# Kernel optimization log

Measured on AMD Instinct MI355X. Metric: run time of the kernel, lower is better.

## Reference

```python
import jax, jax.numpy as jnp
import numpy as np

# Model hyperparameters (match init_kwargs)
T = 3          # reasoning hops
L = 3          # rule channels (parallel LSTMs)
E = 50000      # number of entities
N = 1000000    # number of KG triples
R = 200        # r_size = (n-1)//2
NREL = 2 * R + 1  # n = 401 (forward rels, inverse rels, identity)
H = 256        # emb_size
TAU = 10.0     # tau_1 softmax temperature
TOPK = 1000    # top-k state pruning for hops t>=1
B = 8          # batch size


def setup_inputs() -> dict:
    key = jax.random.key(0)
    ks = jax.random.split(key, 16)
    s = 0.05
    return {
        "input_x": jax.random.randint(ks[0], (B,), 0, E),
        "input_r": jax.random.randint(ks[1], (B,), 0, NREL),
        "e2triple": jax.random.randint(ks[2], (3, N), 0, E),
        "triple2e": jax.random.randint(ks[3], (2, N), 0, E),
        "r2triple": jax.random.randint(ks[4], (1, N), 0, R),
        "emb": jax.random.normal(ks[5], (NREL, H), jnp.float32) * s,
        "Wih_f": jax.random.normal(ks[6], (L, 4 * H, H), jnp.float32) * s,
        "Whh_f": jax.random.normal(ks[7], (L, 4 * H, H), jnp.float32) * s,
        "bih_f": jax.random.normal(ks[8], (L, 4 * H), jnp.float32) * s,
        "bhh_f": jax.random.normal(ks[9], (L, 4 * H), jnp.float32) * s,
        "Wih_b": jax.random.normal(ks[10], (L, 4 * H, H), jnp.float32) * s,
        "Whh_b": jax.random.normal(ks[11], (L, 4 * H, H), jnp.float32) * s,
        "bih_b": jax.random.normal(ks[12], (L, 4 * H), jnp.float32) * s,
        "bhh_b": jax.random.normal(ks[13], (L, 4 * H), jnp.float32) * s,
        "linW": jax.random.normal(ks[14], (NREL, 2 * H), jnp.float32) * s,
        "linb": jax.random.normal(ks[15], (NREL,), jnp.float32) * s,
    }


def _lstm_scan(x, Wih, Whh, bih, bhh):
    # x: [S, B, H]; PyTorch gate order i, f, g, o. Returns hidden seq [S, B, H].
    Bn = x.shape[1]
    Hh = Whh.shape[1]
    pre = x @ Wih.T + bih + bhh  # hoist input projection out of the scan

    def step(carry, xt):
        h, c = carry
        g = xt + h @ Whh.T
        i, f, gg, o = jnp.split(g, 4, axis=-1)
        c = jax.nn.sigmoid(f) * c + jax.nn.sigmoid(i) * jnp.tanh(gg)
        h = jax.nn.sigmoid(o) * jnp.tanh(c)
        return (h, c), h

    init = (jnp.zeros((Bn, Hh), x.dtype), jnp.zeros((Bn, Hh), x.dtype))
    _, hs = jax.lax.scan(step, init, pre)
    return hs


def reference(input_x, input_r, e2triple, triple2e, r2triple, emb,
              Wih_f, Whh_f, bih_f, bhh_f, Wih_b, Whh_b, bih_b, bhh_b,
              linW, linb):
    Bsz = input_x.shape[0]
    x0 = jax.nn.one_hot(input_x, E, dtype=emb.dtype)  # [B, E] one-hot query entity
    q = emb[input_r]                                   # [B, H] query relation emb
    # [T+1, B, H]: T copies of the query rel emb, last step is the special emb[-1]
    seq = jnp.concatenate([
        jnp.broadcast_to(q[None], (T, Bsz, H)),
        jnp.broadcast_to(emb[-1][None, None, :], (1, Bsz, H)),
    ], axis=0)

    outs = []
    for l in range(L):  # small fixed number of structurally distinct LSTMs
        hf = _lstm_scan(seq, Wih_f[l], Whh_f[l], bih_f[l], bhh_f[l])
        hb = _lstm_scan(seq[::-1], Wih_b[l], Whh_b[l], bih_b[l], bhh_b[l])[::-1]
        rnn = jnp.concatenate([hf, hb], axis=-1).transpose(1, 0, 2)  # [B, T+1, 2H]
        outs.append(rnn[:, :-1] @ linW.T + linb)                      # [B, T, n]
    w_all = jnp.stack(outs, axis=2)  # [B, T, L, n]

    heads = e2triple[0]   # [N] head entity per triple
    tails = triple2e[1]   # [N] tail entity per triple
    tails2 = e2triple[2]  # [N] tail entity per triple (inverse-direction gather)
    rels = r2triple[0]    # [N] relation per triple, in [0, R)

    def propagate(x, w):
        # x: [B, *, E] entity state, w: [B, L, n] relation weights
        s_i = w[:, :, -1:] * x                              # identity relation
        msg_f = x[:, :, heads] * w[:, :, rels]              # [B, L, N] fwd messages
        s_h = jnp.zeros((Bsz, L, E), x.dtype).at[:, :, tails].add(msg_f)
        msg_b = x[:, :, tails2] * w[:, :, rels + R]         # inverse relations
        s_t = jnp.zeros((Bsz, L, E), x.dtype).at[:, :, heads].add(msg_b)
        return s_i + s_h + s_t

    def prune_topk(x, k):
        # keep top-k entity scores per (batch, channel), zero the rest
        th = jax.lax.top_k(x, k)[0][..., -1:]
        return jnp.where(x >= th, x, jnp.zeros((), x.dtype))

    s = None
    for t in range(T):
        w = jax.nn.softmax(w_all[:, t] / TAU, axis=-1)      # [B, L, n]
        xin = x0[:, None, :] if t == 0 else prune_topk(s, TOPK)
        st = propagate(xin, w)
        s = st / jnp.maximum(st.sum(-1, keepdims=True), 1e-7)
    return s.sum(axis=1)  # [B, E]
```

## Files before the change

kernel.cpp:

```cpp
#include <hip/hip_runtime.h>
#include <math.h>

#define TT 3
#define LL 3
#define EE 50000
#define NN 1000000
#define RR 200
#define NRELC 401
#define HH 256
#define BB 8
#define KTOP 1000
#define SROW 24
#define NBUCK 782
#define BSH 6
#define CSRN (2 * NN)
#define STB 512
#define SEGS 50176

__device__ __forceinline__ float sigmoidf_(float x) {
    if (x >= 0.f) { return 1.f / (1.f + expf(-x)); }
    float z = expf(x); return z / (1.f + z);
}

__global__ __launch_bounds__(256) void pre_kernel(
    const int* __restrict__ input_r, const float* __restrict__ emb,
    const float* __restrict__ Wih_f, const float* __restrict__ bih_f, const float* __restrict__ bhh_f,
    const float* __restrict__ Wih_b, const float* __restrict__ bih_b, const float* __restrict__ bhh_b,
    float* __restrict__ preq, float* __restrict__ pree)
{
    int wave = blockIdx.x * 4 + (threadIdx.x >> 6);
    if (wave >= 1536) return;
    int lane = threadIdx.x & 63;
    int row0 = wave * 4;
    int ld = row0 >> 10;
    int l = ld >> 1, dir = ld & 1;
    const float* Wih = (dir ? Wih_b : Wih_f) + (size_t)l * 4 * HH * HH;
    const float* bih = (dir ? bih_b : bih_f) + l * 4 * HH;
    const float* bhh = (dir ? bhh_b : bhh_f) + l * 4 * HH;

    float4 xf[9];
    for (int b = 0; b < 8; ++b) {
        int r = input_r[b];
        xf[b] = *(const float4*)(emb + (size_t)r * HH + lane * 4);
    }
    xf[8] = *(const float4*)(emb + (size_t)(NRELC - 1) * HH + lane * 4);

    for (int rr = 0; rr < 4; ++rr) {
        int row = (row0 + rr) & 1023;
        float4 w4 = *(const float4*)(Wih + (size_t)row * HH + lane * 4);
        float acc[9];
        #pragma unroll
        for (int c = 0; c < 9; ++c)
            acc[c] = w4.x * xf[c].x + w4.y * xf[c].y + w4.z * xf[c].z + w4.w * xf[c].w;
        #pragma unroll
        for (int off = 32; off > 0; off >>= 1)
            #pragma unroll
            for (int c = 0; c < 9; ++c) acc[c] += __shfl_xor(acc[c], off);
        float bsum = bih[row] + bhh[row];
        if (lane < 8) preq[((size_t)ld * 8 + lane) * 1024 + row] = acc[lane] + bsum;
        if (lane == 8) pree[(size_t)ld * 1024 + row] = acc[8] + bsum;
    }
}

__global__ __launch_bounds__(256) void rec_kernel(
    const float* __restrict__ Whh_f, const float* __restrict__ Whh_b,
    const float* __restrict__ preq, const float* __restrict__ pree,
    const float* __restrict__ hstate, float* __restrict__ gates, int step)
{
    int wave = blockIdx.x * 4 + (threadIdx.x >> 6);
    if (wave >= 1536) return;
    int lane = threadIdx.x & 63;
    int row0 = wave * 4;
    int ld = row0 >> 10;
    int l = ld >> 1, dir = ld & 1;
    const float* Whh = (dir ? Whh_b : Whh_f) + (size_t)l * 4 * HH * HH;
    bool use_e = dir ? (step == 0) : (step == 3);

    float4 hf[8];
    for (int b = 0; b < 8; ++b)
        hf[b] = *(const float4*)(hstate + ((size_t)ld * 8 + b) * HH + lane * 4);

    for (int rr = 0; rr < 4; ++rr) {
        int row = (row0 + rr) & 1023;
        float4 w4 = *(const float4*)(Whh + (size_t)row * HH + lane * 4);
        float acc[8];
        #pragma unroll
        for (int b = 0; b < 8; ++b)
            acc[b] = w4.x * hf[b].x + w4.y * hf[b].y + w4.z * hf[b].z + w4.w * hf[b].w;
        #pragma unroll
        for (int off = 32; off > 0; off >>= 1)
            #pragma unroll
            for (int b = 0; b < 8; ++b) acc[b] += __shfl_xor(acc[b], off);
        if (lane < 8) {
            float pre = use_e ? pree[(size_t)ld * 1024 + row]
                              : preq[((size_t)ld * 8 + lane) * 1024 + row];
            gates[((size_t)ld * 8 + lane) * 1024 + row] = acc[lane] + pre;
        }
    }
}

__global__ __launch_bounds__(256) void hupdate_kernel(
    const float* __restrict__ preq, const float* __restrict__ pree,
    const float* __restrict__ gates, float* __restrict__ hstate,
    float* __restrict__ cstate, float* __restrict__ hbuf2, int step)
{
    int g = blockIdx.x * 256 + threadIdx.x;
    int ld = g >> 11;
    int b = (g >> 8) & 7;
    int j = g & 255;
    int dir = ld & 1;
    bool use_e = dir ? (step == 0) : (step == 3);
    float gv[4];
    #pragma unroll
    for (int q = 0; q < 4; ++q) {
        int row = q * 256 + j;
        if (step == 0)
            gv[q] = use_e ? pree[(size_t)ld * 1024 + row]
                          : preq[((size_t)ld * 8 + b) * 1024 + row];
        else
            gv[q] = gates[((size_t)ld * 8 + b) * 1024 + row];
    }
    float c = (step == 0) ? 0.f : cstate[g];
    float iv = sigmoidf_(gv[0]), fv = sigmoidf_(gv[1]);
    float gg = tanhf(gv[2]),     ov = sigmoidf_(gv[3]);
    c = fv * c + iv * gg;
    float h = ov * tanhf(c);
    cstate[g] = c;
    hstate[g] = h;
    int t_out = dir ? (3 - step) : step;
    if (t_out <= 2) hbuf2[(((size_t)ld * 8 + b) * 3 + t_out) * HH + j] = h;
}

__global__ __launch_bounds__(256) void logits_dot(
    const float* __restrict__ hbuf2, const float* __restrict__ linW,
    const float* __restrict__ linb, float* __restrict__ wbuf)
{
    int wave = blockIdx.x * 4 + (threadIdx.x >> 6);
    if (wave >= 3 * 3 * NRELC) return;
    int lane = threadIdx.x & 63;
    int n = wave % NRELC;
    int tc = wave / NRELC;
    int t = tc / 3, chunk = tc % 3;
    const float4* wr = (const float4*)(linW + (size_t)n * 2 * HH + lane * 8);
    float4 w4a = wr[0], w4b = wr[1];
    float acc[8];
    #pragma unroll
    for (int i = 0; i < 8; ++i) {
        int combo = chunk * 8 + i;
        int b = combo / 3, l = combo % 3;
        int ldh = (lane < 32) ? (l * 2 + 0) : (l * 2 + 1);
        const float* hsrc = hbuf2 + (((size_t)ldh * 8 + b) * 3 + t) * HH + (lane & 31) * 8;
        float4 f0 = *(const float4*)hsrc;
        float4 f1 = *(const float4*)(hsrc + 4);
        acc[i] = w4a.x * f0.x + w4a.y * f0.y + w4a.z * f0.z + w4a.w * f0.w
               + w4b.x * f1.x + w4b.y * f1.y + w4b.z * f1.z + w4b.w * f1.w;
    }
    #pragma unroll
    for (int off = 32; off > 0; off >>= 1)
        #pragma unroll
        for (int i = 0; i < 8; ++i) acc[i] += __shfl_xor(acc[i], off);
    if (lane < 8) {
        int combo = chunk * 8 + lane;
        wbuf[((size_t)t * 24 + combo) * NRELC + n] = acc[lane] + linb[n];
    }
}

__global__ __launch_bounds__(256) void softmax_kernel(float* __restrict__ wbuf) {
    int rowi = blockIdx.x;
    float* w = wbuf + (size_t)rowi * NRELC;
    __shared__ float red[256];
    int tid = threadIdx.x;
    float v0 = w[tid];
    float v1 = (tid + 256 < NRELC) ? w[tid + 256] : -1e30f;
    red[tid] = fmaxf(v0, v1); __syncthreads();
    for (int s2 = 128; s2 > 0; s2 >>= 1) {
        if (tid < s2) red[tid] = fmaxf(red[tid], red[tid + s2]);
        __syncthreads();
    }
    float m = red[0]; __syncthreads();
    float e0 = expf((v0 - m) * 0.1f);
    float e1 = (tid + 256 < NRELC) ? expf((v1 - m) * 0.1f) : 0.f;
    red[tid] = e0 + e1; __syncthreads();
    for (int s2 = 128; s2 > 0; s2 >>= 1) {
        if (tid < s2) red[tid] += red[tid + s2];
        __syncthreads();
    }
    float denom = red[0];
    w[tid] = e0 / denom;
    if (tid + 256 < NRELC) w[tid + 256] = e1 / denom;
}

__global__ __launch_bounds__(256) void fill_seed(
    float* __restrict__ s, const int* __restrict__ input_x, const float* __restrict__ w0,
    unsigned* __restrict__ rowcnt)
{
    __shared__ int xs[8];
    __shared__ float wv[24];
    if (threadIdx.x < 8) xs[threadIdx.x] = input_x[threadIdx.x];
    if (threadIdx.x < 24) wv[threadIdx.x] = w0[(size_t)threadIdx.x * NRELC + (NRELC - 1)];
    if (blockIdx.x == 0 && threadIdx.x < 24) rowcnt[threadIdx.x] = 0u;
    __syncthreads();
    int i = blockIdx.x * 256 + threadIdx.x;
    if (i >= SROW * EE) return;
    int row = i % 24;
    int e = i / 24;
    s[i] = (e == xs[row / 3]) ? wv[row] : 0.f;
}

__global__ __launch_bounds__(256) void hop0_scan(
    const int* __restrict__ heads, const int* __restrict__ tails,
    const int* __restrict__ tails2, const int* __restrict__ rels,
    const int* __restrict__ input_x, const float* __restrict__ w0,
    float* __restrict__ s)
{
    __shared__ int xs[BB];
    if (threadIdx.x < BB) xs[threadIdx.x] = input_x[threadIdx.x];
    __syncthreads();
    int i = blockIdx.x * 256 + threadIdx.x;
    if (i >= NN) return;
    int h = heads[i], t2 = tails2[i];
    bool any = false;
    #pragma unroll
    for (int b = 0; b < BB; ++b) any = any || (h == xs[b]) || (t2 == xs[b]);
    if (!any) return;
    int tl = tails[i], rr = rels[i];
    for (int b = 0; b < BB; ++b) {
        if (h == xs[b])
            for (int l = 0; l < LL; ++l)
                atomicAdd(&s[(size_t)tl * SROW + b * 3 + l], w0[(b * 3 + l) * NRELC + rr]);
        if (t2 == xs[b])
            for (int l = 0; l < LL; ++l)
                atomicAdd(&s[(size_t)h * SROW + b * 3 + l], w0[(b * 3 + l) * NRELC + rr + RR]);
    }
}

__global__ __launch_bounds__(256) void rowsum_compact(
    const float* __restrict__ s, float* __restrict__ partial,
    unsigned* __restrict__ ckey, unsigned* __restrict__ rowcnt, int do_compact)
{
    __shared__ float acc[24];
    __shared__ unsigned lkey[24][168];
    __shared__ unsigned lcnt[24];
    __shared__ unsigned lbase[24];
    int tid = threadIdx.x;
    if (tid < 24) { acc[tid] = 0.f; lcnt[tid] = 0u; }
    __syncthreads();
    int gidx = blockIdx.x * 256 + tid;
    int row = gidx % 24;
    float a = 0.f;
    const int total = SROW * EE;
    for (int k0 = 0; k0 < 52; k0 += 13) {
        for (int kk = 0; kk < 13; ++kk) {
            long i = (long)gidx + (long)(k0 + kk) * 24576;
            if (i < total) {
                float v = s[i];
                a += v;
                if (do_compact && __float_as_uint(v) != 0u) {
                    unsigned slot = atomicAdd(&lcnt[row], 1u);
                    slot = min(slot, 167u);
                    lkey[row][slot] = __float_as_uint(v);
                }
            }
        }
        if (do_compact) {
            __syncthreads();
            if (tid < 24) {
                unsigned c = min(lcnt[tid], 168u);
                lcnt[tid] = c;
                lbase[tid] = min(atomicAdd(&rowcnt[tid], c), (unsigned)SEGS);
            }
            __syncthreads();
            int r = tid % 24;
            int nthr = (r < 16) ? 11 : 10;
            unsigned cnt = lcnt[r], base = lbase[r];
            if (base + cnt > (unsigned)SEGS) cnt = (unsigned)SEGS - base;
            for (unsigned j = (unsigned)(tid / 24); j < cnt; j += nthr)
                ckey[(size_t)r * SEGS + base + j] = lkey[r][j];
            __syncthreads();
            if (tid < 24) lcnt[tid] = 0u;
            __syncthreads();
        }
    }
    atomicAdd(&acc[row], a);
    __syncthreads();
    if (tid < 24) partial[blockIdx.x * 24 + tid] = acc[tid];
}

__global__ __launch_bounds__(256) void rowsum_fin(
    const float* __restrict__ partial, float* __restrict__ sums,
    const float* __restrict__ w_t, float* __restrict__ wsc,
    float* __restrict__ wTg)
{
    int r = blockIdx.x;
    int tid = threadIdx.x;
    __shared__ float sa;
    if (tid == 0) {
        float a = 0.f;
        for (int j = 0; j < 96; ++j) a += partial[j * 24 + r];
        a = fmaxf(a, 1e-7f);
        sums[r] = a;
        sa = a;
    }
    __syncthreads();
    if (w_t != nullptr) {
        float a = sa;
        for (int i = tid; i < NRELC; i += 256) {
            float v = w_t[(size_t)r * NRELC + i] / a;
            wsc[(size_t)r * NRELC + i] = v;
            if (wTg != nullptr && i < 2 * RR) wTg[(size_t)i * SROW + r] = v;
        }
    }
}

__global__ __launch_bounds__(256) void rowsum_fin2(
    const float* __restrict__ partial2, float* __restrict__ sums,
    const float* __restrict__ w_t, float* __restrict__ wsc,
    float* __restrict__ wTg)
{
    int r = blockIdx.x;
    int tid = threadIdx.x;
    __shared__ float red[256];
    float a = 0.f;
    for (int g = tid; g < NBUCK; g += 256) a += partial2[(size_t)g * 24 + r];
    red[tid] = a; __syncthreads();
    for (int s2 = 128; s2 > 0; s2 >>= 1) {
        if (tid < s2) red[tid] += red[tid + s2];
        __syncthreads();
    }
    __shared__ float sa;
    if (tid == 0) { sa = fmaxf(red[0], 1e-7f); sums[r] = sa; }
    __syncthreads();
    if (w_t != nullptr) {
        float aa = sa;
        for (int i = tid; i < NRELC; i += 256) {
            float v = w_t[(size_t)r * NRELC + i] / aa;
            wsc[(size_t)r * NRELC + i] = v;
            if (wTg != nullptr && i < 2 * RR) wTg[(size_t)i * SROW + r] = v;
        }
    }
}

__global__ __launch_bounds__(512) void topk_select(
    const unsigned* __restrict__ ckey, const unsigned* __restrict__ rowcnt,
    float* __restrict__ th, int* __restrict__ mask)
{
    int row = blockIdx.x, tid = threadIdx.x;
    {
        int per = (EE + 23) / 24;
        int e0 = row * per, e1 = min(e0 + per, EE);
        for (int e = e0 + tid; e < e1; e += 512) mask[e] = 0;
    }
    const unsigned* keys = ckey + (size_t)row * SEGS;
    int n = min((int)rowcnt[row], SEGS);
    __shared__ unsigned hist[256];
    __shared__ int red[256];
    __shared__ int sh_bin, sh_rem;
    unsigned prefix = 0;
    int remk = KTOP;
    int iters = (n + 511) / 512;
    int lane = tid & 63;
    for (int round = 0; round < 4; ++round) {
        if (tid < 256) hist[tid] = 0u;
        __syncthreads();
        int shift = 24 - 8 * round;
        for (int it = 0; it < iters; ++it) {
            int i = it * 512 + tid;
            bool valid = (i < n);
            unsigned key = valid ? keys[i] : 0u;
            valid = valid && (round == 0 || (key >> (shift + 8)) == prefix);
            unsigned bin = valid ? ((key >> shift) & 255u) : 0u;
            unsigned long long peers = __ballot(valid);
            #pragma unroll
            for (int bit = 0; bit < 8; ++bit) {
                unsigned long long bm = __ballot(valid && ((bin >> bit) & 1u));
                peers &= ((bin >> bit) & 1u) ? bm : ~bm;
            }
            if (valid) {
                unsigned long long lower = peers & ((1ull << lane) - 1ull);
                if (lower == 0ull)
                    atomicAdd(&hist[bin], (unsigned)__popcll(peers));
            }
        }
        __syncthreads();
        if (tid < 256) red[tid] = (int)hist[tid];
        __syncthreads();
        for (int off = 1; off < 256; off <<= 1) {
            int v = 0;
            if (tid < 256 && tid + off < 256) v = red[tid + off];
            __syncthreads();
            if (tid < 256) red[tid] += v;
            __syncthreads();
        }
        if (tid == 0) { sh_bin = 0; sh_rem = remk; }
        __syncthreads();
        if (tid < 256) {
            int cnt = (int)hist[tid];
            int above = (tid == 255) ? 0 : red[tid + 1];
            if (above < remk && above + cnt >= remk) { sh_bin = tid; sh_rem = remk - above; }
        }
        __syncthreads();
        prefix = (prefix << 8) | (unsigned)sh_bin;
        remk = sh_rem;
        __syncthreads();
    }
    if (tid == 0) th[row] = __uint_as_float(prefix);
}

__global__ __launch_bounds__(256) void prune_flat(
    float* __restrict__ s, const float* __restrict__ th,
    const float* __restrict__ wsc, float* __restrict__ x, int* __restrict__ mask,
    unsigned* __restrict__ rowcnt, int write_s)
{
    __shared__ float ths[24], w4s[24];
    if (threadIdx.x < 24) {
        ths[threadIdx.x] = th[threadIdx.x];
        w4s[threadIdx.x] = wsc[threadIdx.x * NRELC + (NRELC - 1)];
    }
    if (blockIdx.x == 0 && threadIdx.x < 24) rowcnt[threadIdx.x] = 0u;
    __syncthreads();
    int i = blockIdx.x * 256 + threadIdx.x;
    if (i >= SROW * EE) return;
    int row = i % 24;
    int e = i / 24;
    float v = s[i];
    float xv = (v >= ths[row]) ? v : 0.f;
    x[i] = xv;
    if (write_s) s[i] = w4s[row] * xv;
    if (xv > 0.f) atomicOr(&mask[e], 1 << (row / 3));
}

__global__ __launch_bounds__(256) void hop_scan(
    const int* __restrict__ heads, const int* __restrict__ tails,
    const int* __restrict__ tails2, const int* __restrict__ rels,
    const int* __restrict__ mask, const float* __restrict__ x,
    const float* __restrict__ wsc, float* __restrict__ s)
{
    int gid = blockIdx.x * 256 + threadIdx.x;
    int i = gid >> 3;
    if (i >= NN) return;
    int b = gid & 7;
    int h = heads[i], t2 = tails2[i];
    int mh = mask[h], mt = mask[t2];
    bool ah = (mh >> b) & 1;
    bool at = (mt >> b) & 1;
    if (!(ah || at)) return;
    int tl = tails[i], rr = rels[i];
    int row = b * 3;
    if (ah) {
        float v0 = x[(size_t)h * SROW + row];
        float v1 = x[(size_t)h * SROW + row + 1];
        float v2 = x[(size_t)h * SROW + row + 2];
        if (v0 != 0.f) atomicAdd(&s[(size_t)tl * SROW + row],     v0 * wsc[(row)     * NRELC + rr]);
        if (v1 != 0.f) atomicAdd(&s[(size_t)tl * SROW + row + 1], v1 * wsc[(row + 1) * NRELC + rr]);
        if (v2 != 0.f) atomicAdd(&s[(size_t)tl * SROW + row + 2], v2 * wsc[(row + 2) * NRELC + rr]);
    }
    if (at) {
        float v0 = x[(size_t)t2 * SROW + row];
        float v1 = x[(size_t)t2 * SROW + row + 1];
        float v2 = x[(size_t)t2 * SROW + row + 2];
        if (v0 != 0.f) atomicAdd(&s[(size_t)h * SROW + row],     v0 * wsc[(row)     * NRELC + rr + RR]);
        if (v1 != 0.f) atomicAdd(&s[(size_t)h * SROW + row + 1], v1 * wsc[(row + 1) * NRELC + rr + RR]);
        if (v2 != 0.f) atomicAdd(&s[(size_t)h * SROW + row + 2], v2 * wsc[(row + 2) * NRELC + rr + RR]);
    }
}

__global__ __launch_bounds__(256) void csr_hist(
    const int* __restrict__ heads, const int* __restrict__ tails,
    unsigned* __restrict__ bh)
{
    __shared__ unsigned h[NBUCK];
    int tid = threadIdx.x;
    for (int i = tid; i < NBUCK; i += 256) h[i] = 0u;
    __syncthreads();
    for (int i = blockIdx.x * 256 + tid; i < NN; i += STB * 256) {
        atomicAdd(&h[tails[i] >> BSH], 1u);
        atomicAdd(&h[heads[i] >> BSH], 1u);
    }
    __syncthreads();
    for (int j = tid; j < NBUCK; j += 256)
        bh[(size_t)j * STB + blockIdx.x] = h[j];
}

__global__ __launch_bounds__(512) void csr_scanb(
    unsigned* __restrict__ bh, unsigned* __restrict__ gcnt)
{
    __shared__ unsigned sc[STB];
    int bk = blockIdx.x, tid = threadIdx.x;
    unsigned v = bh[(size_t)bk * STB + tid];
    sc[tid] = v; __syncthreads();
    #pragma unroll
    for (int o = 1; o < STB; o <<= 1) {
        unsigned u = (tid >= o) ? sc[tid - o] : 0u;
        __syncthreads();
        sc[tid] += u;
        __syncthreads();
    }
    bh[(size_t)bk * STB + tid] = sc[tid] - v;
    if (tid == STB - 1) gcnt[bk] = sc[tid];
}

__global__ __launch_bounds__(1024) void csr_scan2(
    const unsigned* __restrict__ gcnt, unsigned* __restrict__ gOff)
{
    __shared__ unsigned sc[1024];
    int tid = threadIdx.x;
    unsigned v = (tid < NBUCK) ? gcnt[tid] : 0u;
    sc[tid] = v; __syncthreads();
    #pragma unroll
    for (int o = 1; o < 1024; o <<= 1) {
        unsigned u = (tid >= o) ? sc[tid - o] : 0u;
        __syncthreads();
        sc[tid] += u;
        __syncthreads();
    }
    if (tid < NBUCK) gOff[tid] = sc[tid] - v;
    if (tid == NBUCK - 1) gOff[NBUCK] = sc[tid];
}

__global__ __launch_bounds__(256) void csr_stage2(
    const int* __restrict__ heads, const int* __restrict__ tails,
    const int* __restrict__ tails2, const int* __restrict__ rels,
    const unsigned* __restrict__ gOff, const unsigned* __restrict__ bh,
    unsigned* __restrict__ staging)
{
    __shared__ unsigned base[NBUCK];
    __shared__ unsigned cur[NBUCK];
    int tid = threadIdx.x;
    for (int j = tid; j < NBUCK; j += 256) {
        base[j] = gOff[j] + bh[(size_t)j * STB + blockIdx.x];
        cur[j] = 0u;
    }
    __syncthreads();
    for (int i = blockIdx.x * 256 + tid; i < NN; i += STB * 256) {
        unsigned rl = (unsigned)rels[i];
        int h = heads[i], d1 = tails[i], t2 = tails2[i];
        unsigned p1 = base[d1 >> BSH] + atomicAdd(&cur[d1 >> BSH], 1u);
        if (p1 < (unsigned)CSRN)
            staging[p1] = ((unsigned)(d1 & 63) << 26) | ((unsigned)h << 9) | rl;
        unsigned p2 = base[h >> BSH] + atomicAdd(&cur[h >> BSH], 1u);
        if (p2 < (unsigned)CSRN)
            staging[p2] = ((unsigned)(h & 63) << 26) | ((unsigned)t2 << 9) | (rl + RR);
    }
}

__global__ __launch_bounds__(256) void hop_bucket(
    const unsigned* __restrict__ gOff, const unsigned* __restrict__ staging,
    const int* __restrict__ mask, const float* __restrict__ x,
    const float* __restrict__ wT, const float* __restrict__ wsc,
    float* __restrict__ s, float* __restrict__ partial2,
    unsigned* __restrict__ ckey, unsigned* __restrict__ rowcnt, int do_compact)
{
    __shared__ float sl[64][24];
    __shared__ float w4s[24];
    __shared__ float acc24[24];
    __shared__ unsigned lcnt[24];
    __shared__ unsigned lbase[24];
    __shared__ unsigned lkey[24][64];
    int bk = blockIdx.x, tid = threadIdx.x;
    for (int i = tid; i < 64 * 24; i += 256) ((float*)sl)[i] = 0.f;
    if (tid < 24) {
        w4s[tid] = wsc[tid * NRELC + (NRELC - 1)];
        acc24[tid] = 0.f;
        lcnt[tid] = 0u;
    }
    __syncthreads();
    unsigned j0 = gOff[bk], j1 = gOff[bk + 1];
    for (unsigned j = j0 + tid; j < j1; j += 256) {
        unsigned p = staging[j];
        int src = (int)((p >> 9) & 0xFFFFu);
        int m = mask[src];
        if (!m) continue;
        int dl = (int)(p >> 26);
        int rel = (int)(p & 511u);
        const float* xs = x + (size_t)src * SROW;
        const float* wr = wT + (size_t)rel * SROW;
        while (m) {
            int b = __ffs(m) - 1; m &= m - 1;
            int r = b * 3;
            atomicAdd(&sl[dl][r],     xs[r]     * wr[r]);
            atomicAdd(&sl[dl][r + 1], xs[r + 1] * wr[r + 1]);
            atomicAdd(&sl[dl][r + 2], xs[r + 2] * wr[r + 2]);
        }
    }
    __syncthreads();
    int e0 = bk * 64;
    for (int idx = tid; idx < 64 * 24; idx += 256) {
        int el = idx / 24, row = idx % 24;
        int e = e0 + el;
        if (e >= EE) continue;
        float v = sl[el][row] + w4s[row] * x[(size_t)e * SROW + row];
        s[(size_t)e * SROW + row] = v;
        atomicAdd(&acc24[row], v);
        if (do_compact && __float_as_uint(v) != 0u) {
            unsigned slot = atomicAdd(&lcnt[row], 1u);
            slot = min(slot, 63u);
            lkey[row][slot] = __float_as_uint(v);
        }
    }
    __syncthreads();
    if (tid < 24) partial2[(size_t)bk * 24 + tid] = acc24[tid];
    if (do_compact) {
        if (tid < 24) {
            unsigned c = min(lcnt[tid], 64u);
            lcnt[tid] = c;
            lbase[tid] = min(atomicAdd(&rowcnt[tid], c), (unsigned)SEGS);
        }
        __syncthreads();
        int r = tid % 24;
        int nthr = (r < 16) ? 11 : 10;
        unsigned cnt = lcnt[r], base = lbase[r];
        if (base + cnt > (unsigned)SEGS) cnt = (unsigned)SEGS - base;
        for (unsigned j = (unsigned)(tid / 24); j < cnt; j += nthr)
            ckey[(size_t)r * SEGS + base + j] = lkey[r][j];
    }
}

__global__ void final_kernel(const float* __restrict__ s, const float* __restrict__ sums,
                             float* __restrict__ out) {
    __shared__ float ss[24];
    if (threadIdx.x < 24) ss[threadIdx.x] = sums[threadIdx.x];
    __syncthreads();
    int e = blockIdx.x * 256 + threadIdx.x;
    if (e >= EE) return;
    const float* se = s + (size_t)e * SROW;
    #pragma unroll
    for (int b = 0; b < 8; ++b)
        out[(size_t)b * EE + e] = se[b * 3] / ss[b * 3]
                                + se[b * 3 + 1] / ss[b * 3 + 1]
                                + se[b * 3 + 2] / ss[b * 3 + 2];
}

extern "C" void kernel_launch(void* const* d_in, const int* in_sizes, int n_in,
                              void* d_out, int out_size, void* d_ws, size_t ws_size,
                              hipStream_t stream)
{
    const int*   input_x  = (const int*)d_in[0];
    const int*   input_r  = (const int*)d_in[1];
    const int*   e2triple = (const int*)d_in[2];
    const int*   triple2e = (const int*)d_in[3];
    const int*   r2triple = (const int*)d_in[4];
    const float* emb      = (const float*)d_in[5];
    const float* Wih_f    = (const float*)d_in[6];
    const float* Whh_f    = (const float*)d_in[7];
    const float* bih_f    = (const float*)d_in[8];
    const float* bhh_f    = (const float*)d_in[9];
    const float* Wih_b    = (const float*)d_in[10];
    const float* Whh_b    = (const float*)d_in[11];
    const float* bih_b    = (const float*)d_in[12];
    const float* bhh_b    = (const float*)d_in[13];
    const float* linW     = (const float*)d_in[14];
    const float* linb     = (const float*)d_in[15];

    const int* heads  = e2triple;
    const int* tails2 = e2triple + 2 * (size_t)NN;
    const int* tails  = triple2e + (size_t)NN;
    const int* rels   = r2triple;

    float* ws      = (float*)d_ws;
    float* hbuf    = ws;
    float* wbuf    = hbuf + 36864;
    float* xst     = wbuf + 28872;
    float* sst     = xst + 1200000;
    float* sums    = sst + 1200000;
    float* th      = sums + 24;
    int*   mask    = (int*)(th + 24);
    float* partial = (float*)(mask + EE);
    unsigned* rowcnt  = (unsigned*)(partial + 2304);
    float* partial2   = (float*)(rowcnt + 32);
    unsigned* ckey    = (unsigned*)(partial2 + NBUCK * 24);
    unsigned* bh      = ckey + 24 * (size_t)SEGS;
    unsigned* gcnt    = bh + (size_t)NBUCK * STB;
    unsigned* gOff    = gcnt + 784;
    unsigned* staging = gOff + 800;
    float*    wT      = (float*)(staging + CSRN);
    const size_t NEED = (size_t)((wT + 9600) - ws) * 4;
    const bool use_csr = (ws_size >= NEED);
    float* wsc    = hbuf;
    float* preq   = xst;
    float* pree   = preq + 49152;
    float* gates  = pree + 6144;
    float* hstate = gates + 49152;
    float* cstate = hstate + 12288;

    float* out = (float*)d_out;
    const int EBLK  = (EE + 255) / 256;
    const int SBLK  = (SROW * EE + 255) / 256;
    const int NBLK  = (NN + 255) / 256;
    const int N8BLK = (NN * 8) / 256;

    pre_kernel<<<384, 256, 0, stream>>>(input_r, emb, Wih_f, bih_f, bhh_f,
                                        Wih_b, bih_b, bhh_b, preq, pree);
    hupdate_kernel<<<48, 256, 0, stream>>>(preq, pree, gates, hstate, cstate, hbuf, 0);
    for (int s = 1; s <= 3; ++s) {
        rec_kernel<<<384, 256, 0, stream>>>(Whh_f, Whh_b, preq, pree, hstate, gates, s);
        hupdate_kernel<<<48, 256, 0, stream>>>(preq, pree, gates, hstate, cstate, hbuf, s);
    }
    logits_dot<<<903, 256, 0, stream>>>(hbuf, linW, linb, wbuf);
    softmax_kernel<<<72, 256, 0, stream>>>(wbuf);

    if (use_csr) {
        csr_hist<<<STB, 256, 0, stream>>>(heads, tails, bh);
        csr_scanb<<<NBUCK, 512, 0, stream>>>(bh, gcnt);
        csr_scan2<<<1, 1024, 0, stream>>>(gcnt, gOff);
        csr_stage2<<<STB, 256, 0, stream>>>(heads, tails, tails2, rels, gOff, bh, staging);
    }

    fill_seed<<<SBLK, 256, 0, stream>>>(sst, input_x, wbuf, rowcnt);
    hop0_scan<<<NBLK, 256, 0, stream>>>(heads, tails, tails2, rels, input_x, wbuf, sst);
    rowsum_compact<<<96, 256, 0, stream>>>(sst, partial, ckey, rowcnt, 1);
    rowsum_fin<<<24, 256, 0, stream>>>(partial, sums, wbuf + 1 * 24 * NRELC, wsc,
                                       use_csr ? wT : nullptr);

    for (int t = 1; t < TT; ++t) {
        topk_select<<<24, 512, 0, stream>>>(ckey, rowcnt, th, mask);
        prune_flat<<<SBLK, 256, 0, stream>>>(sst, th, wsc, xst, mask, rowcnt,
                                             use_csr ? 0 : 1);
        const float* w_next = (t + 1 < TT) ? (wbuf + (size_t)(t + 1) * 24 * NRELC) : nullptr;
        if (use_csr) {
            hop_bucket<<<NBUCK, 256, 0, stream>>>(gOff, staging, mask, xst, wT, wsc,
                                                  sst, partial2, ckey, rowcnt,
                                                  (t + 1 < TT) ? 1 : 0);
            rowsum_fin2<<<24, 256, 0, stream>>>(partial2, sums, w_next, wsc, wT);
        } else {
            hop_scan<<<N8BLK, 256, 0, stream>>>(heads, tails, tails2, rels, mask, xst, wsc, sst);
            rowsum_compact<<<96, 256, 0, stream>>>(sst, partial, ckey, rowcnt,
                                                   (t + 1 < TT) ? 1 : 0);
            rowsum_fin<<<24, 256, 0, stream>>>(partial, sums, w_next, wsc, nullptr);
        }
    }

    final_kernel<<<EBLK, 256, 0, stream>>>(sst, sums, out);
}
```

Before: 323.0 us.

## Fuse LSTM gate update into matvec kernels, merge CSR histogram, widen rowsum grid

The LSTM recurrence now computes all four gates of one hidden unit in a single wave and applies the cell/hidden update in the same kernel. This removes the separate hupdate launches and the gates buffer, and hidden state ping-pongs between two buffers. The CSR histogram runs as extra blocks of the pre-projection kernel so both share one launch. rowsum_compact moves to 384 blocks with a single compaction pass instead of 96 blocks with four passes, which makes the partial-sum reduction longer.

```diff
diff --git a/kernel.cpp b/kernel.cpp
--- a/kernel.cpp
+++ b/kernel.cpp
@@ -22,17 +22,35 @@
     float z = expf(x); return z / (1.f + z);
 }
 
-__global__ __launch_bounds__(256) void pre_kernel(
+__global__ __launch_bounds__(256) void pre_fused(
     const int* __restrict__ input_r, const float* __restrict__ emb,
     const float* __restrict__ Wih_f, const float* __restrict__ bih_f, const float* __restrict__ bhh_f,
     const float* __restrict__ Wih_b, const float* __restrict__ bih_b, const float* __restrict__ bhh_b,
-    float* __restrict__ preq, float* __restrict__ pree)
-{
+    float* __restrict__ preq, float* __restrict__ pree,
+    float* __restrict__ hstate, float* __restrict__ cstate, float* __restrict__ hbuf2,
+    const int* __restrict__ heads, const int* __restrict__ tails,
+    unsigned* __restrict__ bh, int do_hist)
+{
+    if (blockIdx.x >= 384) {
+        if (!do_hist) return;
+        __shared__ unsigned h[NBUCK];
+        int tid = threadIdx.x;
+        int bid = blockIdx.x - 384;
+        for (int i = tid; i < NBUCK; i += 256) h[i] = 0u;
+        __syncthreads();
+        for (int i = bid * 256 + tid; i < NN; i += STB * 256) {
+            atomicAdd(&h[tails[i] >> BSH], 1u);
+            atomicAdd(&h[heads[i] >> BSH], 1u);
+        }
+        __syncthreads();
+        for (int j = tid; j < NBUCK; j += 256)
+            bh[(size_t)j * STB + bid] = h[j];
+        return;
+    }
     int wave = blockIdx.x * 4 + (threadIdx.x >> 6);
-    if (wave >= 1536) return;
     int lane = threadIdx.x & 63;
-    int row0 = wave * 4;
-    int ld = row0 >> 10;
+    int ld = wave >> 8;
+    int j  = wave & 255;
     int l = ld >> 1, dir = ld & 1;
     const float* Wih = (dir ? Wih_b : Wih_f) + (size_t)l * 4 * HH * HH;
     const float* bih = (dir ? bih_b : bih_f) + l * 4 * HH;
@@ -45,8 +63,9 @@
     }
     xf[8] = *(const float4*)(emb + (size_t)(NRELC - 1) * HH + lane * 4);
 
-    for (int rr = 0; rr < 4; ++rr) {
-        int row = (row0 + rr) & 1023;
+    float g4[4], ge4[4];
+    for (int q = 0; q < 4; ++q) {
+        int row = q * 256 + j;
         float4 w4 = *(const float4*)(Wih + (size_t)row * HH + lane * 4);
         float acc[9];
         #pragma unroll
@@ -57,31 +76,44 @@
             #pragma unroll
             for (int c = 0; c < 9; ++c) acc[c] += __shfl_xor(acc[c], off);
         float bsum = bih[row] + bhh[row];
-        if (lane < 8) preq[((size_t)ld * 8 + lane) * 1024 + row] = acc[lane] + bsum;
-        if (lane == 8) pree[(size_t)ld * 1024 + row] = acc[8] + bsum;
-    }
-}
-
-__global__ __launch_bounds__(256) void rec_kernel(
+        g4[q]  = (lane < 8 ? acc[lane] : 0.f) + bsum;
+        ge4[q] = acc[8] + bsum;
+        if (lane < 8) preq[((size_t)ld * 8 + lane) * 1024 + row] = g4[q];
+        if (lane == 8) pree[(size_t)ld * 1024 + row] = ge4[q];
+    }
+    if (lane < 8) {
+        float gi, gg, go;
+        if (dir == 0) { gi = g4[0]; gg = g4[2]; go = g4[3]; }
+        else          { gi = ge4[0]; gg = ge4[2]; go = ge4[3]; }
+        float c = sigmoidf_(gi) * tanhf(gg);
+        float h = sigmoidf_(go) * tanhf(c);
+        int g = (ld * 8 + lane) * 256 + j;
+        cstate[g] = c;
+        hstate[g] = h;
+        if (dir == 0) hbuf2[(((size_t)ld * 8 + lane) * 3 + 0) * HH + j] = h;
+    }
+}
+
+__global__ __launch_bounds__(256) void rec_fused(
     const float* __restrict__ Whh_f, const float* __restrict__ Whh_b,
     const float* __restrict__ preq, const float* __restrict__ pree,
-    const float* __restrict__ hstate, float* __restrict__ gates, int step)
+    const float* __restrict__ hprev, float* __restrict__ hnext,
+    float* __restrict__ cstate, float* __restrict__ hbuf2, int step)
 {
     int wave = blockIdx.x * 4 + (threadIdx.x >> 6);
-    if (wave >= 1536) return;
     int lane = threadIdx.x & 63;
-    int row0 = wave * 4;
-    int ld = row0 >> 10;
+    int ld = wave >> 8, j = wave & 255;
     int l = ld >> 1, dir = ld & 1;
     const float* Whh = (dir ? Whh_b : Whh_f) + (size_t)l * 4 * HH * HH;
-    bool use_e = dir ? (step == 0) : (step == 3);
+    bool use_e = (dir == 0) && (step == 3);
 
     float4 hf[8];
     for (int b = 0; b < 8; ++b)
-        hf[b] = *(const float4*)(hstate + ((size_t)ld * 8 + b) * HH + lane * 4);
-
-    for (int rr = 0; rr < 4; ++rr) {
-        int row = (row0 + rr) & 1023;
+        hf[b] = *(const float4*)(hprev + ((size_t)ld * 8 + b) * HH + lane * 4);
+
+    float g4[4];
+    for (int q = 0; q < 4; ++q) {
+        int row = q * 256 + j;
         float4 w4 = *(const float4*)(Whh + (size_t)row * HH + lane * 4);
         float acc[8];
         #pragma unroll
@@ -94,41 +126,21 @@
         if (lane < 8) {
             float pre = use_e ? pree[(size_t)ld * 1024 + row]
                               : preq[((size_t)ld * 8 + lane) * 1024 + row];
-            gates[((size_t)ld * 8 + lane) * 1024 + row] = acc[lane] + pre;
-        }
-    }
-}
-
-__global__ __launch_bounds__(256) void hupdate_kernel(
-    const float* __restrict__ preq, const float* __restrict__ pree,
-    const float* __restrict__ gates, float* __restrict__ hstate,
-    float* __restrict__ cstate, float* __restrict__ hbuf2, int step)
-{
-    int g = blockIdx.x * 256 + threadIdx.x;
-    int ld = g >> 11;
-    int b = (g >> 8) & 7;
-    int j = g & 255;
-    int dir = ld & 1;
-    bool use_e = dir ? (step == 0) : (step == 3);
-    float gv[4];
-    #pragma unroll
-    for (int q = 0; q < 4; ++q) {
-        int row = q * 256 + j;
-        if (step == 0)
-            gv[q] = use_e ? pree[(size_t)ld * 1024 + row]
-                          : preq[((size_t)ld * 8 + b) * 1024 + row];
-        else
-            gv[q] = gates[((size_t)ld * 8 + b) * 1024 + row];
-    }
-    float c = (step == 0) ? 0.f : cstate[g];
-    float iv = sigmoidf_(gv[0]), fv = sigmoidf_(gv[1]);
-    float gg = tanhf(gv[2]),     ov = sigmoidf_(gv[3]);
-    c = fv * c + iv * gg;
-    float h = ov * tanhf(c);
-    cstate[g] = c;
-    hstate[g] = h;
-    int t_out = dir ? (3 - step) : step;
-    if (t_out <= 2) hbuf2[(((size_t)ld * 8 + b) * 3 + t_out) * HH + j] = h;
+            g4[q] = acc[lane] + pre;
+        }
+    }
+    if (lane < 8) {
+        int g = (ld * 8 + lane) * 256 + j;
+        float c = cstate[g];
+        float iv = sigmoidf_(g4[0]), fv = sigmoidf_(g4[1]);
+        float gg = tanhf(g4[2]),     ov = sigmoidf_(g4[3]);
+        c = fv * c + iv * gg;
+        float h = ov * tanhf(c);
+        cstate[g] = c;
+        hnext[g] = h;
+        int t_out = dir ? (3 - step) : step;
+        if (t_out <= 2) hbuf2[(((size_t)ld * 8 + lane) * 3 + t_out) * HH + j] = h;
+    }
 }
 
 __global__ __launch_bounds__(256) void logits_dot(
@@ -249,37 +261,33 @@
     int row = gidx % 24;
     float a = 0.f;
     const int total = SROW * EE;
-    for (int k0 = 0; k0 < 52; k0 += 13) {
-        for (int kk = 0; kk < 13; ++kk) {
-            long i = (long)gidx + (long)(k0 + kk) * 24576;
-            if (i < total) {
-                float v = s[i];
-                a += v;
-                if (do_compact && __float_as_uint(v) != 0u) {
-                    unsigned slot = atomicAdd(&lcnt[row], 1u);
-                    slot = min(slot, 167u);
-                    lkey[row][slot] = __float_as_uint(v);
-                }
+    for (int k = 0; k < 13; ++k) {
+        long i = (long)gidx + (long)k * 98304;
+        if (i < total) {
+            float v = s[i];
+            a += v;
+            if (do_compact && __float_as_uint(v) != 0u) {
+                unsigned slot = atomicAdd(&lcnt[row], 1u);
+                slot = min(slot, 167u);
+                lkey[row][slot] = __float_as_uint(v);
             }
         }
-        if (do_compact) {
-            __syncthreads();
-            if (tid < 24) {
-                unsigned c = min(lcnt[tid], 168u);
-                lcnt[tid] = c;
-                lbase[tid] = min(atomicAdd(&rowcnt[tid], c), (unsigned)SEGS);
-            }
-            __syncthreads();
-            int r = tid % 24;
-            int nthr = (r < 16) ? 11 : 10;
-            unsigned cnt = lcnt[r], base = lbase[r];
-            if (base + cnt > (unsigned)SEGS) cnt = (unsigned)SEGS - base;
-            for (unsigned j = (unsigned)(tid / 24); j < cnt; j += nthr)
-                ckey[(size_t)r * SEGS + base + j] = lkey[r][j];
-            __syncthreads();
-            if (tid < 24) lcnt[tid] = 0u;
-            __syncthreads();
-        }
+    }
+    if (do_compact) {
+        __syncthreads();
+        if (tid < 24) {
+            unsigned c = min(lcnt[tid], 168u);
+            lcnt[tid] = c;
+            lbase[tid] = min(atomicAdd(&rowcnt[tid], c), (unsigned)SEGS);
+        }
+        __syncthreads();
+        int r = tid % 24;
+        int nthr = (r < 16) ? 11 : 10;
+        unsigned cnt = lcnt[r], base = lbase[r];
+        if (base + cnt > (unsigned)SEGS) cnt = (unsigned)SEGS - base;
+        for (unsigned j = (unsigned)(tid / 24); j < cnt; j += nthr)
+            ckey[(size_t)r * SEGS + base + j] = lkey[r][j];
+        __syncthreads();
     }
     atomicAdd(&acc[row], a);
     __syncthreads();
@@ -296,7 +304,7 @@
     __shared__ float sa;
     if (tid == 0) {
         float a = 0.f;
-        for (int j = 0; j < 96; ++j) a += partial[j * 24 + r];
+        for (int j = 0; j < 384; ++j) a += partial[j * 24 + r];
         a = fmaxf(a, 1e-7f);
         sums[r] = a;
         sa = a;
@@ -464,23 +472,6 @@
     }
 }
 
-__global__ __launch_bounds__(256) void csr_hist(
-    const int* __restrict__ heads, const int* __restrict__ tails,
-    unsigned* __restrict__ bh)
-{
-    __shared__ unsigned h[NBUCK];
-    int tid = threadIdx.x;
-    for (int i = tid; i < NBUCK; i += 256) h[i] = 0u;
-    __syncthreads();
-    for (int i = blockIdx.x * 256 + tid; i < NN; i += STB * 256) {
-        atomicAdd(&h[tails[i] >> BSH], 1u);
-        atomicAdd(&h[heads[i] >> BSH], 1u);
-    }
-    __syncthreads();
-    for (int j = tid; j < NBUCK; j += 256)
-        bh[(size_t)j * STB + blockIdx.x] = h[j];
-}
-
 __global__ __launch_bounds__(512) void csr_scanb(
     unsigned* __restrict__ bh, unsigned* __restrict__ gcnt)
 {
@@ -665,7 +656,7 @@
     float* th      = sums + 24;
     int*   mask    = (int*)(th + 24);
     float* partial = (float*)(mask + EE);
-    unsigned* rowcnt  = (unsigned*)(partial + 2304);
+    unsigned* rowcnt  = (unsigned*)(partial + 9216);
     float* partial2   = (float*)(rowcnt + 32);
     unsigned* ckey    = (unsigned*)(partial2 + NBUCK * 24);
     unsigned* bh      = ckey + 24 * (size_t)SEGS;
@@ -675,12 +666,12 @@
     float*    wT      = (float*)(staging + CSRN);
     const size_t NEED = (size_t)((wT + 9600) - ws) * 4;
     const bool use_csr = (ws_size >= NEED);
-    float* wsc    = hbuf;
-    float* preq   = xst;
-    float* pree   = preq + 49152;
-    float* gates  = pree + 6144;
-    float* hstate = gates + 49152;
-    float* cstate = hstate + 12288;
+    float* wsc     = hbuf;
+    float* preq    = xst;
+    float* pree    = preq + 49152;
+    float* hstateA = pree + 6144;
+    float* hstateB = hstateA + 12288;
+    float* cstate  = hstateB + 12288;
 
     float* out = (float*)d_out;
     const int EBLK  = (EE + 255) / 256;
@@ -688,18 +679,20 @@
     const int NBLK  = (NN + 255) / 256;
     const int N8BLK = (NN * 8) / 256;
 
-    pre_kernel<<<384, 256, 0, stream>>>(input_r, emb, Wih_f, bih_f, bhh_f,
-                                        Wih_b, bih_b, bhh_b, preq, pree);
-    hupdate_kernel<<<48, 256, 0, stream>>>(preq, pree, gates, hstate, cstate, hbuf, 0);
-    for (int s = 1; s <= 3; ++s) {
-        rec_kernel<<<384, 256, 0, stream>>>(Whh_f, Whh_b, preq, pree, hstate, gates, s);
-        hupdate_kernel<<<48, 256, 0, stream>>>(preq, pree, gates, hstate, cstate, hbuf, s);
-    }
+    pre_fused<<<896, 256, 0, stream>>>(input_r, emb, Wih_f, bih_f, bhh_f,
+                                       Wih_b, bih_b, bhh_b, preq, pree,
+                                       hstateA, cstate, hbuf,
+                                       heads, tails, bh, use_csr ? 1 : 0);
+    rec_fused<<<384, 256, 0, stream>>>(Whh_f, Whh_b, preq, pree, hstateA, hstateB,
+                                       cstate, hbuf, 1);
+    rec_fused<<<384, 256, 0, stream>>>(Whh_f, Whh_b, preq, pree, hstateB, hstateA,
+                                       cstate, hbuf, 2);
+    rec_fused<<<384, 256, 0, stream>>>(Whh_f, Whh_b, preq, pree, hstateA, hstateB,
+                                       cstate, hbuf, 3);
     logits_dot<<<903, 256, 0, stream>>>(hbuf, linW, linb, wbuf);
     softmax_kernel<<<72, 256, 0, stream>>>(wbuf);
 
     if (use_csr) {
-        csr_hist<<<STB, 256, 0, stream>>>(heads, tails, bh);
         csr_scanb<<<NBUCK, 512, 0, stream>>>(bh, gcnt);
         csr_scan2<<<1, 1024, 0, stream>>>(gcnt, gOff);
         csr_stage2<<<STB, 256, 0, stream>>>(heads, tails, tails2, rels, gOff, bh, staging);
@@ -707,7 +700,7 @@
 
     fill_seed<<<SBLK, 256, 0, stream>>>(sst, input_x, wbuf, rowcnt);
     hop0_scan<<<NBLK, 256, 0, stream>>>(heads, tails, tails2, rels, input_x, wbuf, sst);
-    rowsum_compact<<<96, 256, 0, stream>>>(sst, partial, ckey, rowcnt, 1);
+    rowsum_compact<<<384, 256, 0, stream>>>(sst, partial, ckey, rowcnt, 1);
     rowsum_fin<<<24, 256, 0, stream>>>(partial, sums, wbuf + 1 * 24 * NRELC, wsc,
                                        use_csr ? wT : nullptr);
 
@@ -723,8 +716,8 @@
             rowsum_fin2<<<24, 256, 0, stream>>>(partial2, sums, w_next, wsc, wT);
         } else {
             hop_scan<<<N8BLK, 256, 0, stream>>>(heads, tails, tails2, rels, mask, xst, wsc, sst);
-            rowsum_compact<<<96, 256, 0, stream>>>(sst, partial, ckey, rowcnt,
-                                                   (t + 1 < TT) ? 1 : 0);
+            rowsum_compact<<<384, 256, 0, stream>>>(sst, partial, ckey, rowcnt,
+                                                    (t + 1 < TT) ? 1 : 0);
             rowsum_fin<<<24, 256, 0, stream>>>(partial, sums, w_next, wsc, nullptr);
         }
     }
```

Result: faster. 316.3 us (-2.1%).
